# Kernel optimization log

Measured on AMD Instinct MI355X. Metric: run time of the kernel, lower is better.

Reference implementation:

```python
import jax, jax.numpy as jnp
import numpy as np

B, T, E, H = 2, 4096, 1024, 16
D = E // H  # head dim = 64

def setup_inputs() -> dict:
    key = jax.random.key(0)
    ks = jax.random.split(key, 5)
    x = jax.random.normal(ks[0], (B, T, E), dtype=jnp.float32)
    # torch Linear(n_embed, 3*n_embed): y = x @ W.T + b ; we store W already transposed as (E, 3E)
    w_qkv = jax.random.normal(ks[1], (E, 3 * E), dtype=jnp.float32) * (1.0 / np.sqrt(E))
    b_qkv = jax.random.normal(ks[2], (3 * E,), dtype=jnp.float32) * 0.02
    w_out = jax.random.normal(ks[3], (E, E), dtype=jnp.float32) * (1.0 / np.sqrt(E))
    b_out = jax.random.normal(ks[4], (E,), dtype=jnp.float32) * 0.02
    return {"x": x, "w_qkv": w_qkv, "b_qkv": b_qkv, "w_out": w_out, "b_out": b_out}

def reference(x, w_qkv, b_qkv, w_out, b_out):
    b, t, e = x.shape
    qkv = x @ w_qkv + b_qkv                      # (B,T,3E)
    # matches torch: view(B,T,H,3D) then chunk(3, dim=-1)
    qkv = qkv.reshape(b, t, H, 3 * D)
    q, k, v = jnp.split(qkv, 3, axis=-1)          # each (B,T,H,D)
    q = q.transpose(0, 2, 1, 3)                   # (B,H,T,D)
    k = k.transpose(0, 2, 1, 3)
    v = v.transpose(0, 2, 1, 3)
    scores = jnp.einsum('bhqd,bhkd->bhqk', q, k) / jnp.sqrt(jnp.float32(D))
    causal = jnp.tril(jnp.ones((t, t), dtype=bool))
    scores = jnp.where(causal, scores, jnp.float32(-jnp.inf))
    w = jax.nn.softmax(scores, axis=-1)           # (B,H,T,T)
    out = jnp.einsum('bhqk,bhkd->bhqd', w, v)     # (B,H,T,D)
    out = out.transpose(0, 2, 1, 3).reshape(b, t, e)
    return out @ w_out + b_out
```

## Files before the change

### kernel.cpp

```cpp
#include <hip/hip_runtime.h>
#include <stdint.h>
#include <math.h>

#define T_SEQ 4096

typedef __attribute__((ext_vector_type(8))) short short8;
typedef __attribute__((ext_vector_type(4))) float f32x4;
typedef __attribute__((ext_vector_type(4))) uint16_t u16x4;

__device__ __forceinline__ uint16_t f2bf(float f) {
  uint32_t u = __float_as_uint(f);
  u += 0x7FFFu + ((u >> 16) & 1u);
  return (uint16_t)(u >> 16);
}

__device__ __forceinline__ void gload_lds16(const uint16_t* g, uint16_t* l) {
  __builtin_amdgcn_global_load_lds(
      (const __attribute__((address_space(1))) void*)g,
      (__attribute__((address_space(3))) void*)l, 16, 0, 0);
}

__global__ void __launch_bounds__(256) k_cvt(const float* __restrict__ in,
                                             uint16_t* __restrict__ out, int n4) {
  int i = blockIdx.x * 256 + threadIdx.x;
  if (i >= n4) return;
  float4 v = reinterpret_cast<const float4*>(in)[i];
  u16x4 o = { f2bf(v.x), f2bf(v.y), f2bf(v.z), f2bf(v.w) };
  reinterpret_cast<u16x4*>(out)[i] = o;
}

__global__ void __launch_bounds__(256) k_tc(const float* __restrict__ w,
                                            uint16_t* __restrict__ wt, int R, int C) {
  __shared__ uint16_t tile[32][33];
  int tx = threadIdx.x & 31, ty = threadIdx.x >> 5;
  int r0 = blockIdx.y * 32, c0 = blockIdx.x * 32;
#pragma unroll
  for (int i = 0; i < 4; i++)
    tile[ty + 8 * i][tx] = f2bf(w[(size_t)(r0 + ty + 8 * i) * C + c0 + tx]);
  __syncthreads();
#pragma unroll
  for (int i = 0; i < 4; i++)
    wt[(size_t)(c0 + ty + 8 * i) * R + r0 + tx] = tile[tx][ty + 8 * i];
}

__global__ void __launch_bounds__(256) k_vt(const uint16_t* __restrict__ qkv,
                                            uint16_t* __restrict__ vT) {
  __shared__ uint16_t tile[64][65];
  const int bh = blockIdx.y, b = bh >> 4, h = bh & 15;
  const int t0 = blockIdx.x * 64;
  const int tid = threadIdx.x;
  const int r = tid >> 3, c8 = tid & 7;
  const uint16_t* src = qkv + ((size_t)b * T_SEQ + t0) * 3072 + h * 192 + 128;
#pragma unroll
  for (int i = 0; i < 2; i++) {
    int row = r + 32 * i;
    short8 v = *reinterpret_cast<const short8*>(src + (size_t)row * 3072 + c8 * 8);
#pragma unroll
    for (int j = 0; j < 8; j++) tile[row][c8 * 8 + j] = (uint16_t)v[j];
  }
  __syncthreads();
  uint16_t* dst = vT + ((size_t)bh * 64) * T_SEQ + t0;
#pragma unroll
  for (int i = 0; i < 2; i++) {
    int d = r + 32 * i;
    short8 v;
#pragma unroll
    for (int j = 0; j < 8; j++) v[j] = (short)tile[c8 * 8 + j][d];
    *reinterpret_cast<short8*>(dst + (size_t)d * T_SEQ + c8 * 8) = v;
  }
}

template <int BF16_OUT>
__global__ void __launch_bounds__(256, 2) k_gemm(const uint16_t* __restrict__ A,
                                                 const uint16_t* __restrict__ BT,
                                                 const float* __restrict__ bias,
                                                 void* __restrict__ Cout,
                                                 int M, int N, int K) {
  __shared__ __align__(16) uint16_t As[2][128 * 64];
  __shared__ __align__(16) uint16_t Bs[2][128 * 64];
  const int tid = threadIdx.x;
  const int lane = tid & 63, wid = tid >> 6;
  const int lr = lane & 15, lg = lane >> 4;
  const int wr = wid >> 1, wc = wid & 1;

  const int bid = blockIdx.x;
  const int cpx = gridDim.x >> 3;
  const int lin = (bid & 7) * cpx + (bid >> 3);
  const int mt = M >> 7;
  const int n0 = (lin / mt) * 128;
  const int m0 = (lin % mt) * 128;

  const f32x4 vzero = {0.f, 0.f, 0.f, 0.f};
  f32x4 acc[4][4];
#pragma unroll
  for (int i = 0; i < 4; i++)
#pragma unroll
    for (int j = 0; j < 4; j++) acc[i][j] = vzero;

  const int sl = lane >> 3, ss = lane & 7;
  const int swzs = (ss ^ sl) * 8;
  const uint16_t* a0 = A + (size_t)(m0 + wid * 32 + sl) * K + swzs;
  const uint16_t* b0 = BT + (size_t)(n0 + wid * 32 + sl) * K + swzs;
  const size_t r8 = (size_t)8 * K;

#define STAGE(bsel, t)                                                   \
  do {                                                                   \
    const int koff_ = (t) * 64;                                          \
    gload_lds16(a0 + koff_,          &As[bsel][(wid * 32 + 0) * 64]);    \
    gload_lds16(a0 + r8 + koff_,     &As[bsel][(wid * 32 + 8) * 64]);    \
    gload_lds16(a0 + 2 * r8 + koff_, &As[bsel][(wid * 32 + 16) * 64]);   \
    gload_lds16(a0 + 3 * r8 + koff_, &As[bsel][(wid * 32 + 24) * 64]);   \
    gload_lds16(b0 + koff_,          &Bs[bsel][(wid * 32 + 0) * 64]);    \
    gload_lds16(b0 + r8 + koff_,     &Bs[bsel][(wid * 32 + 8) * 64]);    \
    gload_lds16(b0 + 2 * r8 + koff_, &Bs[bsel][(wid * 32 + 16) * 64]);   \
    gload_lds16(b0 + 3 * r8 + koff_, &Bs[bsel][(wid * 32 + 24) * 64]);   \
  } while (0)

  const int nt = K >> 6;
  const int fsw = lr & 7;
  STAGE(0, 0);
  STAGE(1, 1);
  __syncthreads();

  for (int t = 0; t < nt; ++t) {
    const int cur = t & 1;
#pragma unroll
    for (int ks = 0; ks < 2; ++ks) {
      const int col = (((ks * 4 + lg) ^ fsw) * 8);
      short8 af[4], bf[4];
#pragma unroll
      for (int mi = 0; mi < 4; ++mi)
        af[mi] = *reinterpret_cast<const short8*>(
            &As[cur][(wr * 64 + mi * 16 + lr) * 64 + col]);
#pragma unroll
      for (int nj = 0; nj < 4; ++nj)
        bf[nj] = *reinterpret_cast<const short8*>(
            &Bs[cur][(wc * 64 + nj * 16 + lr) * 64 + col]);
      __builtin_amdgcn_s_setprio(1);
#pragma unroll
      for (int mi = 0; mi < 4; ++mi)
#pragma unroll
        for (int nj = 0; nj < 4; ++nj)
          acc[mi][nj] = __builtin_amdgcn_mfma_f32_16x16x32_bf16(af[mi], bf[nj], acc[mi][nj], 0, 0, 0);
      __builtin_amdgcn_s_setprio(0);
    }
    __syncthreads();
    if (t + 2 < nt) STAGE(cur, t + 2);
  }
#undef STAGE

#pragma unroll
  for (int nj = 0; nj < 4; nj++) {
    int col = n0 + wc * 64 + nj * 16 + lr;
    float bv = bias[col];
#pragma unroll
    for (int mi = 0; mi < 4; mi++) {
      int rowb = m0 + wr * 64 + mi * 16 + lg * 4;
#pragma unroll
      for (int r = 0; r < 4; r++) {
        float v = acc[mi][nj][r] + bv;
        if (BF16_OUT)
          ((uint16_t*)Cout)[(size_t)(rowb + r) * N + col] = f2bf(v);
        else
          ((float*)Cout)[(size_t)(rowb + r) * N + col] = v;
      }
    }
  }
}

#define KVB 64
__global__ void __launch_bounds__(256) k_attn(const uint16_t* __restrict__ qkv,
                                              const uint16_t* __restrict__ vT,
                                              uint16_t* __restrict__ out) {
  __shared__ __align__(16) char lds[40960];
  const int tid = threadIdx.x;
  const int lane = tid & 63, wid = tid >> 6;
  const int lr = lane & 15, lg = lane >> 4;
  char* psb = lds + 32768 + wid * 2048;

  const int bid = blockIdx.x;
  const int xcd = bid & 7, j = bid >> 3;
  const int bh = xcd * 4 + (j & 3);
  const int qt = 31 - (j >> 2);
  const int b = bh >> 4, h = bh & 15;
  const int q0 = qt * 128;
  const size_t rowbase = (size_t)b * T_SEQ;
  const int hoff = h * 192;
  const uint16_t* Kg = qkv + rowbase * 3072 + hoff + 64;
  const uint16_t* Vg = vT + (size_t)bh * 64 * T_SEQ;

  const int sr = tid >> 3, sc = tid & 7;
  const int wsw = (sc ^ (sr & 7)) * 16;
  const int swz = (lr & 7) << 4;
  const float C_SC = 0.180336881f;

  short8 ones8;
#pragma unroll
  for (int i = 0; i < 8; i++) ones8[i] = (lr == 0) ? (short)0x3F80 : (short)0;

  const f32x4 vzero = {0.f, 0.f, 0.f, 0.f};

  short8 qf[2][2];
#pragma unroll
  for (int qq = 0; qq < 2; qq++)
#pragma unroll
    for (int c = 0; c < 2; c++) {
      short8 raw = *reinterpret_cast<const short8*>(
          qkv + (rowbase + q0 + wid * 32 + qq * 16 + lr) * 3072 + hoff + c * 32 + lg * 8);
      union { short8 s; uint32_t u[4]; } pk;
#pragma unroll
      for (int e = 0; e < 4; e++) {
        float f0 = __uint_as_float(((uint32_t)(uint16_t)raw[2 * e]) << 16) * C_SC;
        float f1 = __uint_as_float(((uint32_t)(uint16_t)raw[2 * e + 1]) << 16) * C_SC;
        asm("v_cvt_pk_bf16_f32 %0, %1, %2" : "=v"(pk.u[e]) : "v"(f0), "v"(f1));
      }
      qf[qq][c] = pk.s;
    }

  f32x4 o[2][4];
  f32x4 o4[2];
#pragma unroll
  for (int qq = 0; qq < 2; qq++) {
    o4[qq] = vzero;
#pragma unroll
    for (int dt = 0; dt < 4; dt++) o[qq][dt] = vzero;
  }

  const int nkt = 2 * qt + 2;
  const int qwmax = q0 + wid * 32 + 31;

  short8 rk0, rk1, rv0, rv1;
  rk0 = *reinterpret_cast<const short8*>(Kg + (size_t)sr * 3072 + sc * 8);
  rk1 = *reinterpret_cast<const short8*>(Kg + (size_t)(sr + 32) * 3072 + sc * 8);
  rv0 = *reinterpret_cast<const short8*>(Vg + (size_t)sr * T_SEQ + sc * 8);
  rv1 = *reinterpret_cast<const short8*>(Vg + (size_t)(sr + 32) * T_SEQ + sc * 8);
  {
    char* kb0 = lds;
    char* vb0 = lds + 16384;
    *reinterpret_cast<short8*>(kb0 + sr * 128 + wsw) = rk0;
    *reinterpret_cast<short8*>(kb0 + (sr + 32) * 128 + wsw) = rk1;
    *reinterpret_cast<short8*>(vb0 + sr * 128 + wsw) = rv0;
    *reinterpret_cast<short8*>(vb0 + (sr + 32) * 128 + wsw) = rv1;
  }
  if (nkt > 1) {
    rk0 = *reinterpret_cast<const short8*>(Kg + (size_t)(KVB + sr) * 3072 + sc * 8);
    rk1 = *reinterpret_cast<const short8*>(Kg + (size_t)(KVB + sr + 32) * 3072 + sc * 8);
    rv0 = *reinterpret_cast<const short8*>(Vg + (size_t)sr * T_SEQ + KVB + sc * 8);
    rv1 = *reinterpret_cast<const short8*>(Vg + (size_t)(sr + 32) * T_SEQ + KVB + sc * 8);
  }

  for (int kt = 0; kt < nkt; kt++) {
    __syncthreads();
    if (kt + 1 < nkt) {
      const int nsel = (kt + 1) & 1;
      char* kb = lds + (nsel ? 8192 : 0);
      char* vb = lds + 16384 + (nsel ? 8192 : 0);
      *reinterpret_cast<short8*>(kb + sr * 128 + wsw) = rk0;
      *reinterpret_cast<short8*>(kb + (sr + 32) * 128 + wsw) = rk1;
      *reinterpret_cast<short8*>(vb + sr * 128 + wsw) = rv0;
      *reinterpret_cast<short8*>(vb + (sr + 32) * 128 + wsw) = rv1;
      if (kt + 2 < nkt) {
        int k0n = (kt + 2) * KVB;
        rk0 = *reinterpret_cast<const short8*>(Kg + (size_t)(k0n + sr) * 3072 + sc * 8);
        rk1 = *reinterpret_cast<const short8*>(Kg + (size_t)(k0n + sr + 32) * 3072 + sc * 8);
        rv0 = *reinterpret_cast<const short8*>(Vg + (size_t)sr * T_SEQ + k0n + sc * 8);
        rv1 = *reinterpret_cast<const short8*>(Vg + (size_t)(sr + 32) * T_SEQ + k0n + sc * 8);
      }
    }

    if (kt * KVB <= qwmax) {
      const int csel = kt & 1;
      char* kcur = lds + (csel ? 8192 : 0);
      char* vcur = lds + 16384 + (csel ? 8192 : 0);
      f32x4 s0[4], s1[4];
      __builtin_amdgcn_s_setprio(1);
#pragma unroll
      for (int t = 0; t < 4; t++) {
        int row = t * 16 + lr;
        short8 kf0 = *reinterpret_cast<const short8*>(
            kcur + row * 128 + ((lg * 16) ^ swz));
        short8 kf1 = *reinterpret_cast<const short8*>(
            kcur + row * 128 + ((64 + lg * 16) ^ swz));
        s0[t] = __builtin_amdgcn_mfma_f32_16x16x32_bf16(kf0, qf[0][0], vzero, 0, 0, 0);
        s0[t] = __builtin_amdgcn_mfma_f32_16x16x32_bf16(kf1, qf[0][1], s0[t], 0, 0, 0);
        s1[t] = __builtin_amdgcn_mfma_f32_16x16x32_bf16(kf0, qf[1][0], vzero, 0, 0, 0);
        s1[t] = __builtin_amdgcn_mfma_f32_16x16x32_bf16(kf1, qf[1][1], s1[t], 0, 0, 0);
      }
      __builtin_amdgcn_s_setprio(0);
      short8 vf[4][2];
#pragma unroll
      for (int dt = 0; dt < 4; dt++)
#pragma unroll
        for (int c2 = 0; c2 < 2; c2++)
          vf[dt][c2] = *reinterpret_cast<const short8*>(
              vcur + (dt * 16 + lr) * 128 + ((c2 * 64 + lg * 16) ^ swz));

#pragma unroll
      for (int qq = 0; qq < 2; qq++) {
        f32x4* s = qq ? s1 : s0;
        const int qrow = q0 + wid * 32 + qq * 16 + lr;
        const bool notfull = (kt * KVB + 63 > q0 + wid * 32 + qq * 16);
#pragma unroll
        for (int t = 0; t < 4; t++)
#pragma unroll
          for (int r = 0; r < 4; r++) {
            float v = s[t][r];
            if (notfull) {
              int key = kt * KVB + t * 16 + lg * 4 + r;
              if (key > qrow) v = -INFINITY;
            }
            s[t][r] = __builtin_amdgcn_exp2f(v);
          }
#pragma unroll
        for (int t = 0; t < 4; t++) {
          uint32_t w0, w1;
          asm("v_cvt_pk_bf16_f32 %0, %1, %2" : "=v"(w0) : "v"(s[t][0]), "v"(s[t][1]));
          asm("v_cvt_pk_bf16_f32 %0, %1, %2" : "=v"(w1) : "v"(s[t][2]), "v"(s[t][3]));
          uint2 ww; ww.x = w0; ww.y = w1;
          *reinterpret_cast<uint2*>(psb + lr * 128 + ((t * 32 + lg * 8) ^ swz)) = ww;
        }
        __builtin_amdgcn_s_setprio(1);
#pragma unroll
        for (int c2 = 0; c2 < 2; c2++) {
          short8 pf = *reinterpret_cast<const short8*>(
              psb + lr * 128 + ((c2 * 64 + lg * 16) ^ swz));
          o4[qq] = __builtin_amdgcn_mfma_f32_16x16x32_bf16(ones8, pf, o4[qq], 0, 0, 0);
#pragma unroll
          for (int dt = 0; dt < 4; dt++)
            o[qq][dt] = __builtin_amdgcn_mfma_f32_16x16x32_bf16(vf[dt][c2], pf, o[qq][dt], 0, 0, 0);
        }
        __builtin_amdgcn_s_setprio(0);
      }
    }
  }

  __syncthreads();
  char* scrb = lds + wid * 4096;
#pragma unroll
  for (int qq = 0; qq < 2; qq++) {
    float lsum = __shfl(o4[qq][0], lr);
    float inv = 1.0f / lsum;
#pragma unroll
    for (int dt = 0; dt < 4; dt++)
#pragma unroll
      for (int r = 0; r < 4; r++)
        *reinterpret_cast<float*>(scrb + lr * 256 + ((dt * 64 + lg * 16) ^ swz) + r * 4) =
            o[qq][dt][r] * inv;
    int row = lane >> 2, ch = lane & 3;
    uint16_t tmp[16];
#pragma unroll
    for (int k = 0; k < 4; k++) {
      f32x4 vv = *reinterpret_cast<const f32x4*>(
          scrb + row * 256 + ((ch * 64 + k * 16) ^ ((row & 7) << 4)));
#pragma unroll
      for (int j2 = 0; j2 < 4; j2++) tmp[k * 4 + j2] = f2bf(vv[j2]);
    }
    uint16_t* op = out + (rowbase + q0 + wid * 32 + qq * 16 + row) * 1024 + h * 64 + ch * 16;
    *reinterpret_cast<short8*>(op) = *reinterpret_cast<const short8*>(tmp);
    *reinterpret_cast<short8*>(op + 8) = *reinterpret_cast<const short8*>(tmp + 8);
  }
}

extern "C" void kernel_launch(void* const* d_in, const int* in_sizes, int n_in,
                              void* d_out, int out_size, void* d_ws, size_t ws_size,
                              hipStream_t stream) {
  const float* x = (const float*)d_in[0];
  const float* w_qkv = (const float*)d_in[1];
  const float* b_qkv = (const float*)d_in[2];
  const float* w_out = (const float*)d_in[3];
  const float* b_out = (const float*)d_in[4];
  float* out = (float*)d_out;

  uint8_t* ws = (uint8_t*)d_ws;
  uint16_t* x_bf  = (uint16_t*)(ws);
  uint16_t* wqkvT = (uint16_t*)(ws + (16u << 20));
  uint16_t* woutT = (uint16_t*)(ws + (22u << 20));
  uint16_t* qkv   = (uint16_t*)(ws + (24u << 20));
  uint16_t* vTbuf = (uint16_t*)(ws + (72u << 20));
  uint16_t* attn_o = x_bf;

  k_cvt<<<8192, 256, 0, stream>>>(x, x_bf, 2097152);
  k_tc<<<dim3(96, 32), 256, 0, stream>>>(w_qkv, wqkvT, 1024, 3072);
  k_tc<<<dim3(32, 32), 256, 0, stream>>>(w_out, woutT, 1024, 1024);
  k_gemm<1><<<1536, 256, 0, stream>>>(x_bf, wqkvT, b_qkv, qkv, 8192, 3072, 1024);
  k_vt<<<dim3(64, 32), 256, 0, stream>>>(qkv, vTbuf);
  k_attn<<<1024, 256, 0, stream>>>(qkv, vTbuf, attn_o);
  k_gemm<0><<<512, 256, 0, stream>>>(attn_o, woutT, b_out, out, 8192, 1024, 1024);
}
```

Measured before the change: 248.6 us.

## Switch attention to 32x32x16 MFMA with in-register P via permlane32 swap

Rewrites the attention inner loop to use 32x32x16 bf16 MFMAs instead of 16x16x32. The softmax probabilities are rearranged in registers with v_permlane32_swap instead of a round trip through an LDS scratch buffer. The row sum is accumulated in scalar registers plus a cross-half shuffle, replacing the extra ones-vector MFMA. This removes per-tile LDS writes and reads, the extra MFMA work, and shrinks LDS use; the cost is larger accumulator register pressure and a more intricate fragment layout.

```diff
diff --git a/kernel.cpp b/kernel.cpp
--- a/kernel.cpp
+++ b/kernel.cpp
@@ -6,6 +6,7 @@
 
 typedef __attribute__((ext_vector_type(8))) short short8;
 typedef __attribute__((ext_vector_type(4))) float f32x4;
+typedef __attribute__((ext_vector_type(16))) float f32x16;
 typedef __attribute__((ext_vector_type(4))) uint16_t u16x4;
 
 __device__ __forceinline__ uint16_t f2bf(float f) {
@@ -172,11 +173,11 @@
 __global__ void __launch_bounds__(256) k_attn(const uint16_t* __restrict__ qkv,
                                               const uint16_t* __restrict__ vT,
                                               uint16_t* __restrict__ out) {
-  __shared__ __align__(16) char lds[40960];
+  __shared__ __align__(16) char lds[32768];
   const int tid = threadIdx.x;
   const int lane = tid & 63, wid = tid >> 6;
-  const int lr = lane & 15, lg = lane >> 4;
-  char* psb = lds + 32768 + wid * 2048;
+  const int l31 = lane & 31, hi = lane >> 5;
+  const int hi4 = hi * 4;
 
   const int bid = blockIdx.x;
   const int xcd = bid & 7, j = bid >> 3;
@@ -191,40 +192,34 @@
 
   const int sr = tid >> 3, sc = tid & 7;
   const int wsw = (sc ^ (sr & 7)) * 16;
-  const int swz = (lr & 7) << 4;
   const float C_SC = 0.180336881f;
 
-  short8 ones8;
-#pragma unroll
-  for (int i = 0; i < 8; i++) ones8[i] = (lr == 0) ? (short)0x3F80 : (short)0;
-
-  const f32x4 vzero = {0.f, 0.f, 0.f, 0.f};
-
-  short8 qf[2][2];
-#pragma unroll
-  for (int qq = 0; qq < 2; qq++)
-#pragma unroll
-    for (int c = 0; c < 2; c++) {
-      short8 raw = *reinterpret_cast<const short8*>(
-          qkv + (rowbase + q0 + wid * 32 + qq * 16 + lr) * 3072 + hoff + c * 32 + lg * 8);
-      union { short8 s; uint32_t u[4]; } pk;
-#pragma unroll
-      for (int e = 0; e < 4; e++) {
-        float f0 = __uint_as_float(((uint32_t)(uint16_t)raw[2 * e]) << 16) * C_SC;
-        float f1 = __uint_as_float(((uint32_t)(uint16_t)raw[2 * e + 1]) << 16) * C_SC;
-        asm("v_cvt_pk_bf16_f32 %0, %1, %2" : "=v"(pk.u[e]) : "v"(f0), "v"(f1));
-      }
-      qf[qq][c] = pk.s;
-    }
-
-  f32x4 o[2][4];
-  f32x4 o4[2];
-#pragma unroll
-  for (int qq = 0; qq < 2; qq++) {
-    o4[qq] = vzero;
-#pragma unroll
-    for (int dt = 0; dt < 4; dt++) o[qq][dt] = vzero;
-  }
+  int rslot[4];
+#pragma unroll
+  for (int c = 0; c < 4; c++) rslot[c] = (((2 * c + hi) ^ (lane & 7)) << 4);
+  const int rowb128 = l31 * 128;
+
+  const int qrow = q0 + wid * 32 + l31;
+  short8 qf[4];
+#pragma unroll
+  for (int ks = 0; ks < 4; ks++) {
+    short8 raw = *reinterpret_cast<const short8*>(
+        qkv + (rowbase + qrow) * 3072 + hoff + hi * 8 + ks * 16);
+    union { short8 s; uint32_t u[4]; } pk;
+#pragma unroll
+    for (int e = 0; e < 4; e++) {
+      float f0 = __uint_as_float(((uint32_t)(uint16_t)raw[2 * e]) << 16) * C_SC;
+      float f1 = __uint_as_float(((uint32_t)(uint16_t)raw[2 * e + 1]) << 16) * C_SC;
+      asm("v_cvt_pk_bf16_f32 %0, %1, %2" : "=v"(pk.u[e]) : "v"(f0), "v"(f1));
+    }
+    qf[ks] = pk.s;
+  }
+
+  f32x16 o0, o1, zero16;
+#pragma unroll
+  for (int i = 0; i < 16; i++) zero16[i] = 0.f;
+  o0 = zero16; o1 = zero16;
+  float lpart = 0.f;
 
   const int nkt = 2 * qt + 2;
   const int qwmax = q0 + wid * 32 + 31;
@@ -272,92 +267,94 @@
       const int csel = kt & 1;
       char* kcur = lds + (csel ? 8192 : 0);
       char* vcur = lds + 16384 + (csel ? 8192 : 0);
-      f32x4 s0[4], s1[4];
+      const int ktb = kt * KVB;
+      const bool notfull = (ktb + 63 > q0 + wid * 32);
+
+      f32x16 s0 = zero16, s1 = zero16;
       __builtin_amdgcn_s_setprio(1);
 #pragma unroll
-      for (int t = 0; t < 4; t++) {
-        int row = t * 16 + lr;
-        short8 kf0 = *reinterpret_cast<const short8*>(
-            kcur + row * 128 + ((lg * 16) ^ swz));
-        short8 kf1 = *reinterpret_cast<const short8*>(
-            kcur + row * 128 + ((64 + lg * 16) ^ swz));
-        s0[t] = __builtin_amdgcn_mfma_f32_16x16x32_bf16(kf0, qf[0][0], vzero, 0, 0, 0);
-        s0[t] = __builtin_amdgcn_mfma_f32_16x16x32_bf16(kf1, qf[0][1], s0[t], 0, 0, 0);
-        s1[t] = __builtin_amdgcn_mfma_f32_16x16x32_bf16(kf0, qf[1][0], vzero, 0, 0, 0);
-        s1[t] = __builtin_amdgcn_mfma_f32_16x16x32_bf16(kf1, qf[1][1], s1[t], 0, 0, 0);
+      for (int ks = 0; ks < 4; ks++) {
+        short8 kf0 = *reinterpret_cast<const short8*>(kcur + rowb128 + rslot[ks]);
+        short8 kf1 = *reinterpret_cast<const short8*>(kcur + 4096 + rowb128 + rslot[ks]);
+        s0 = __builtin_amdgcn_mfma_f32_32x32x16_bf16(kf0, qf[ks], s0, 0, 0, 0);
+        s1 = __builtin_amdgcn_mfma_f32_32x32x16_bf16(kf1, qf[ks], s1, 0, 0, 0);
       }
       __builtin_amdgcn_s_setprio(0);
-      short8 vf[4][2];
-#pragma unroll
-      for (int dt = 0; dt < 4; dt++)
-#pragma unroll
-        for (int c2 = 0; c2 < 2; c2++)
-          vf[dt][c2] = *reinterpret_cast<const short8*>(
-              vcur + (dt * 16 + lr) * 128 + ((c2 * 64 + lg * 16) ^ swz));
-
-#pragma unroll
-      for (int qq = 0; qq < 2; qq++) {
-        f32x4* s = qq ? s1 : s0;
-        const int qrow = q0 + wid * 32 + qq * 16 + lr;
-        const bool notfull = (kt * KVB + 63 > q0 + wid * 32 + qq * 16);
-#pragma unroll
-        for (int t = 0; t < 4; t++)
-#pragma unroll
-          for (int r = 0; r < 4; r++) {
-            float v = s[t][r];
-            if (notfull) {
-              int key = kt * KVB + t * 16 + lg * 4 + r;
-              if (key > qrow) v = -INFINITY;
-            }
-            s[t][r] = __builtin_amdgcn_exp2f(v);
-          }
-#pragma unroll
-        for (int t = 0; t < 4; t++) {
-          uint32_t w0, w1;
-          asm("v_cvt_pk_bf16_f32 %0, %1, %2" : "=v"(w0) : "v"(s[t][0]), "v"(s[t][1]));
-          asm("v_cvt_pk_bf16_f32 %0, %1, %2" : "=v"(w1) : "v"(s[t][2]), "v"(s[t][3]));
-          uint2 ww; ww.x = w0; ww.y = w1;
-          *reinterpret_cast<uint2*>(psb + lr * 128 + ((t * 32 + lg * 8) ^ swz)) = ww;
-        }
-        __builtin_amdgcn_s_setprio(1);
-#pragma unroll
-        for (int c2 = 0; c2 < 2; c2++) {
-          short8 pf = *reinterpret_cast<const short8*>(
-              psb + lr * 128 + ((c2 * 64 + lg * 16) ^ swz));
-          o4[qq] = __builtin_amdgcn_mfma_f32_16x16x32_bf16(ones8, pf, o4[qq], 0, 0, 0);
-#pragma unroll
-          for (int dt = 0; dt < 4; dt++)
-            o[qq][dt] = __builtin_amdgcn_mfma_f32_16x16x32_bf16(vf[dt][c2], pf, o[qq][dt], 0, 0, 0);
-        }
-        __builtin_amdgcn_s_setprio(0);
+
+      uint32_t u0[8], u1[8];
+#define SMAX_KB(SV, KB, U)                                                    \
+  do {                                                                        \
+    _Pragma("unroll")                                                         \
+    for (int r = 0; r < 16; r++) {                                            \
+      float v = SV[r];                                                        \
+      if (notfull) {                                                          \
+        int key = ktb + (KB) * 32 + (r & 3) + 8 * (r >> 2) + hi4;             \
+        if (key > qrow) v = -INFINITY;                                        \
+      }                                                                       \
+      float p = __builtin_amdgcn_exp2f(v);                                    \
+      SV[r] = p;                                                              \
+      lpart += p;                                                             \
+    }                                                                         \
+    _Pragma("unroll")                                                         \
+    for (int jj = 0; jj < 8; jj++)                                            \
+      asm("v_cvt_pk_bf16_f32 %0, %1, %2"                                      \
+          : "=v"(U[jj]) : "v"(SV[2 * jj]), "v"(SV[2 * jj + 1]));              \
+    asm volatile("v_permlane32_swap_b32 %0, %1" : "+v"(U[0]), "+v"(U[2]));    \
+    asm volatile("v_permlane32_swap_b32 %0, %1" : "+v"(U[1]), "+v"(U[3]));    \
+    asm volatile("v_permlane32_swap_b32 %0, %1" : "+v"(U[4]), "+v"(U[6]));    \
+    asm volatile("v_permlane32_swap_b32 %0, %1" : "+v"(U[5]), "+v"(U[7]));    \
+  } while (0)
+
+      SMAX_KB(s0, 0, u0);
+      SMAX_KB(s1, 1, u1);
+#undef SMAX_KB
+
+      union { uint32_t u[4]; short8 s; } pf;
+      __builtin_amdgcn_s_setprio(1);
+#pragma unroll
+      for (int kv = 0; kv < 4; kv++) {
+        if (kv == 0) { pf.u[0] = u0[0]; pf.u[1] = u0[1]; pf.u[2] = u0[2]; pf.u[3] = u0[3]; }
+        else if (kv == 1) { pf.u[0] = u0[4]; pf.u[1] = u0[5]; pf.u[2] = u0[6]; pf.u[3] = u0[7]; }
+        else if (kv == 2) { pf.u[0] = u1[0]; pf.u[1] = u1[1]; pf.u[2] = u1[2]; pf.u[3] = u1[3]; }
+        else { pf.u[0] = u1[4]; pf.u[1] = u1[5]; pf.u[2] = u1[6]; pf.u[3] = u1[7]; }
+        short8 vf0 = *reinterpret_cast<const short8*>(vcur + rowb128 + rslot[kv]);
+        short8 vf1 = *reinterpret_cast<const short8*>(vcur + 4096 + rowb128 + rslot[kv]);
+        o0 = __builtin_amdgcn_mfma_f32_32x32x16_bf16(vf0, pf.s, o0, 0, 0, 0);
+        o1 = __builtin_amdgcn_mfma_f32_32x32x16_bf16(vf1, pf.s, o1, 0, 0, 0);
       }
+      __builtin_amdgcn_s_setprio(0);
     }
   }
 
   __syncthreads();
-  char* scrb = lds + wid * 4096;
-#pragma unroll
-  for (int qq = 0; qq < 2; qq++) {
-    float lsum = __shfl(o4[qq][0], lr);
-    float inv = 1.0f / lsum;
-#pragma unroll
-    for (int dt = 0; dt < 4; dt++)
-#pragma unroll
-      for (int r = 0; r < 4; r++)
-        *reinterpret_cast<float*>(scrb + lr * 256 + ((dt * 64 + lg * 16) ^ swz) + r * 4) =
-            o[qq][dt][r] * inv;
-    int row = lane >> 2, ch = lane & 3;
-    uint16_t tmp[16];
-#pragma unroll
-    for (int k = 0; k < 4; k++) {
+  float ltot = lpart + __shfl_xor(lpart, 32);
+  float inv = 1.0f / ltot;
+  char* scrb = lds + wid * 8192;
+#pragma unroll
+  for (int g = 0; g < 4; g++) {
+    f32x4 w0, w1;
+#pragma unroll
+    for (int e = 0; e < 4; e++) { w0[e] = o0[4 * g + e] * inv; w1[e] = o1[4 * g + e] * inv; }
+    int s0i = 2 * g + hi, s1i = s0i + 8;
+    *reinterpret_cast<f32x4*>(scrb + l31 * 256 + ((s0i ^ (l31 & 7)) << 4)) = w0;
+    *reinterpret_cast<f32x4*>(scrb + l31 * 256 + ((s1i ^ (l31 & 7)) << 4)) = w1;
+  }
+  asm volatile("s_waitcnt lgkmcnt(0)" ::: "memory");
+  __builtin_amdgcn_sched_barrier(0);
+  {
+    int row = lane >> 1, half = lane & 1;
+    uint16_t tmp[32];
+#pragma unroll
+    for (int k = 0; k < 8; k++) {
       f32x4 vv = *reinterpret_cast<const f32x4*>(
-          scrb + row * 256 + ((ch * 64 + k * 16) ^ ((row & 7) << 4)));
-#pragma unroll
-      for (int j2 = 0; j2 < 4; j2++) tmp[k * 4 + j2] = f2bf(vv[j2]);
-    }
-    uint16_t* op = out + (rowbase + q0 + wid * 32 + qq * 16 + row) * 1024 + h * 64 + ch * 16;
-    *reinterpret_cast<short8*>(op) = *reinterpret_cast<const short8*>(tmp);
-    *reinterpret_cast<short8*>(op + 8) = *reinterpret_cast<const short8*>(tmp + 8);
+          scrb + row * 256 + (((half * 8 + k) ^ (row & 7)) << 4));
+#pragma unroll
+      for (int e = 0; e < 4; e++) tmp[k * 4 + e] = f2bf(vv[e]);
+    }
+    uint16_t* op = out + (rowbase + q0 + wid * 32 + row) * 1024 + h * 64 + half * 32;
+#pragma unroll
+    for (int k = 0; k < 4; k++)
+      *reinterpret_cast<short8*>(op + k * 8) = *reinterpret_cast<const short8*>(tmp + k * 8);
   }
 }
 
```

New measurement: 228.2 us (median of 3 runs). 1.09x faster.
